# Kernel optimization log

Hardware: AMD Instinct MI355X
Metric: run time of the kernel (lower is better)

The kernel has to match this reference:

```python
import jax, jax.numpy as jnp
import numpy as np

D_MODEL = 1024
HEADS = 16
HEAD_DIM = D_MODEL // HEADS


def setup_inputs() -> dict:
    key = jax.random.key(0)
    ks = jax.random.split(key, 9)
    s = 1.0 / np.sqrt(D_MODEL)
    inp = {
        "inputs": jax.random.normal(ks[0], (4, 2048, D_MODEL), dtype=jnp.float32),
        "Wq": jax.random.normal(ks[1], (D_MODEL, D_MODEL), dtype=jnp.float32) * s,
        "bq": jnp.zeros((D_MODEL,), dtype=jnp.float32),
        "Wk": jax.random.normal(ks[2], (D_MODEL, D_MODEL), dtype=jnp.float32) * s,
        "bk": jnp.zeros((D_MODEL,), dtype=jnp.float32),
        "Wv": jax.random.normal(ks[3], (D_MODEL, D_MODEL), dtype=jnp.float32) * s,
        "bv": jnp.zeros((D_MODEL,), dtype=jnp.float32),
        "Wo": jax.random.normal(ks[4], (D_MODEL, D_MODEL), dtype=jnp.float32) * s,
        "bo": jnp.zeros((D_MODEL,), dtype=jnp.float32),
    }
    return inp


def reference(inputs, Wq, bq, Wk, bk, Wv, bv, Wo, bo):
    bs, seq, _ = inputs.shape
    # projections -> [b, h, s, d]
    def split_heads(x):
        return x.reshape(bs, seq, HEADS, HEAD_DIM).transpose(0, 2, 1, 3)
    q = split_heads(inputs @ Wq + bq)
    k = split_heads(inputs @ Wk + bk)
    v = split_heads(inputs @ Wv + bv)
    # NOTE: original code divides by (head_dim ** 1 / 2) == head_dim/2, not sqrt(head_dim)
    scale = HEAD_DIM / 2.0
    scores = jnp.einsum("bhqd,bhkd->bhqk", q, k) / scale
    attn = jax.nn.softmax(scores, axis=-1)
    out = jnp.einsum("bhqk,bhkd->bhqd", attn, v)
    out = out.transpose(0, 2, 1, 3).reshape(bs, seq, HEADS * HEAD_DIM)
    return out @ Wo + bo
```

## Files before the change

### kernel.cpp

```cpp
#include <hip/hip_runtime.h>
#include <stdint.h>

typedef __attribute__((ext_vector_type(8))) short bf16x8;
typedef __attribute__((ext_vector_type(4))) float f32x4;
typedef __attribute__((address_space(1))) void as1_void;
typedef __attribute__((address_space(3))) void as3_void;

#define D_MODEL 1024
#define SEQ     2048
#define BATCH   4
#define HEADS   16
#define HDIM    64

#define QSCALE 0.045084220029218407f

__device__ __forceinline__ ushort f2bf(float f) {
  union { float f; unsigned u; } v; v.f = f;
  unsigned u = v.u + 0x7fffu + ((v.u >> 16) & 1u);
  return (ushort)(u >> 16);
}

__device__ __forceinline__ void gload_lds16(const void* g, void* l) {
  __builtin_amdgcn_global_load_lds((as1_void*)(uintptr_t)g, (as3_void*)l, 16, 0, 0);
}

__device__ __forceinline__ bf16x8 pack8(float a0, float a1, float a2, float a3,
                                        float a4, float a5, float a6, float a7) {
  union { uint u[4]; bf16x8 v; } x;
  x.u[0] = __builtin_amdgcn_perm(__float_as_uint(a1), __float_as_uint(a0), 0x07060302);
  x.u[1] = __builtin_amdgcn_perm(__float_as_uint(a3), __float_as_uint(a2), 0x07060302);
  x.u[2] = __builtin_amdgcn_perm(__float_as_uint(a5), __float_as_uint(a4), 0x07060302);
  x.u[3] = __builtin_amdgcn_perm(__float_as_uint(a7), __float_as_uint(a6), 0x07060302);
  return x.v;
}

__global__ void prep_kernel(const float* __restrict__ X,
                            const float* w0, const float* w1, const float* w2, const float* w3,
                            const float* __restrict__ bq, const float* __restrict__ bk,
                            const float* __restrict__ bv,
                            ushort* __restrict__ Xb, ushort* __restrict__ WT,
                            float* __restrict__ bcat) {
  __shared__ float tile[32][33];
  const int bx = blockIdx.x, t = threadIdx.x;
  if (bx < 8192) {
    int i = bx * 256 + t;
    float4 f = reinterpret_cast<const float4*>(X)[i];
    ushort4 o;
    o.x = f2bf(f.x); o.y = f2bf(f.y); o.z = f2bf(f.z); o.w = f2bf(f.w);
    reinterpret_cast<ushort4*>(Xb)[i] = o;
  } else if (bx < 12288) {
    int tz = bx - 8192;
    int z = tz >> 10;
    int xy = tz & 1023;
    int bxt = xy & 31, byt = xy >> 5;
    const float* w = (z == 0) ? w0 : (z == 1) ? w1 : (z == 2) ? w2 : w3;
    const float sc = (z == 0) ? QSCALE : 1.0f;
    ushort* o = WT + (size_t)z * D_MODEL * D_MODEL;
    int tx = t & 31, ty = t >> 5;
    int x = bxt * 32 + tx;
    int y0 = byt * 32;
    #pragma unroll
    for (int i = ty; i < 32; i += 8)
      tile[i][tx] = w[(size_t)(y0 + i) * D_MODEL + x];
    __syncthreads();
    #pragma unroll
    for (int i = ty; i < 32; i += 8)
      o[(size_t)(bxt * 32 + i) * D_MODEL + y0 + tx] = f2bf(tile[tx][i] * sc);
  } else {
    int i = (bx - 12288) * 256 + t;
    bcat[i] = (i < 1024) ? bq[i] * QSCALE : (i < 2048) ? bk[i - 1024] : bv[i - 2048];
  }
}

#define MFMA16(a, b, c) __builtin_amdgcn_mfma_f32_16x16x32_bf16(a, b, c, 0, 0, 0)

__global__ __launch_bounds__(512, 2) void gemm_qkv(const ushort* __restrict__ A, const ushort* __restrict__ BT,
                                                   const float* __restrict__ bias,
                                                   ushort* __restrict__ QK, ushort* __restrict__ Vt) {
  __shared__ __align__(16) char smem[131072];
  const int tid  = threadIdx.x;
  const int w    = tid >> 6;
  const int lane = tid & 63;
  const int lo   = lane & 15, quad = lane >> 4;
  const int wr   = w >> 2, wc = w & 3;

  const int orig = blockIdx.y * 12 + blockIdx.x;
  const int wg   = (orig & 7) * 48 + (orig >> 3);
  const int m0   = (wg / 12) * 256;
  const int n0   = (wg % 12) * 256;

  const int tl = tid ^ ((tid >> 3) & 7);
  const ushort* sA = A  + (size_t)(m0 + (tl >> 3)) * 1024 + (tl & 7) * 8;
  const ushort* sB = BT + (size_t)(n0 + (tl >> 3)) * 1024 + (tl & 7) * 8;
  char* lw = smem + w * 1024;

  const int o0 = (quad * 16) ^ ((lo & 7) << 4);
  const int o1 = o0 ^ 64;
  const int rdA = wr * 16384 + lo * 128;
  const int rdB = 65536 + (wc * 64 + lo) * 128;

  f32x4 acc[8][4];
  #pragma unroll
  for (int i = 0; i < 8; ++i)
    #pragma unroll
    for (int j = 0; j < 4; ++j) acc[i][j] = {0.f, 0.f, 0.f, 0.f};

  gload_lds16(sB,              lw + 65536);
  gload_lds16(sB +  64 * 1024, lw + 65536 +  8192);
  gload_lds16(sB + 128 * 1024, lw + 65536 + 16384);
  gload_lds16(sB + 192 * 1024, lw + 65536 + 24576);
  gload_lds16(sA,              lw);
  gload_lds16(sA + 128 * 1024, lw + 16384);
  gload_lds16(sA +  64 * 1024, lw +  8192);
  gload_lds16(sA + 192 * 1024, lw + 24576);
  asm volatile("s_waitcnt vmcnt(2)" ::: "memory");
  __builtin_amdgcn_s_barrier();
  asm volatile("" ::: "memory");

  const char* L = smem;
  #pragma unroll 2
  for (int kt = 0; kt < 16; ++kt) {
    const int b32 = (kt & 1) << 15;
    const int nb  = b32 ^ 32768;
    const int kc  = (kt + 1) * 64;
    const bool pf = kt < 15;
    bf16x8 bfr[4][2], af0[2], af1[2];

    #pragma unroll
    for (int ni = 0; ni < 4; ++ni) {
      bfr[ni][0] = *(const bf16x8*)(L + b32 + rdB + ni * 2048 + o0);
      bfr[ni][1] = *(const bf16x8*)(L + b32 + rdB + ni * 2048 + o1);
    }
    af0[0] = *(const bf16x8*)(L + b32 + rdA + o0);
    af0[1] = *(const bf16x8*)(L + b32 + rdA + o1);
    af1[0] = *(const bf16x8*)(L + b32 + rdA + 2048 + o0);
    af1[1] = *(const bf16x8*)(L + b32 + rdA + 2048 + o1);
    if (pf) {
      gload_lds16(sB + kc,             lw + nb + 65536);
      gload_lds16(sB + 64 * 1024 + kc, lw + nb + 65536 + 8192);
    }
    asm volatile("s_waitcnt lgkmcnt(8)" ::: "memory");
    __builtin_amdgcn_s_barrier();
    asm volatile("s_waitcnt lgkmcnt(0)" ::: "memory");
    __builtin_amdgcn_sched_barrier(0);
    __builtin_amdgcn_s_setprio(1);
    #pragma unroll
    for (int ks = 0; ks < 2; ++ks)
      #pragma unroll
      for (int ni = 0; ni < 4; ++ni) {
        acc[0][ni] = MFMA16(af0[ks], bfr[ni][ks], acc[0][ni]);
        acc[1][ni] = MFMA16(af1[ks], bfr[ni][ks], acc[1][ni]);
      }
    __builtin_amdgcn_s_setprio(0);
    __builtin_amdgcn_s_barrier();
    asm volatile("" ::: "memory");

    af0[0] = *(const bf16x8*)(L + b32 + rdA + 2 * 2048 + o0);
    af0[1] = *(const bf16x8*)(L + b32 + rdA + 2 * 2048 + o1);
    af1[0] = *(const bf16x8*)(L + b32 + rdA + 3 * 2048 + o0);
    af1[1] = *(const bf16x8*)(L + b32 + rdA + 3 * 2048 + o1);
    if (pf) {
      gload_lds16(sB + 128 * 1024 + kc, lw + nb + 65536 + 16384);
      gload_lds16(sB + 192 * 1024 + kc, lw + nb + 65536 + 24576);
    }
    __builtin_amdgcn_s_barrier();
    asm volatile("s_waitcnt lgkmcnt(0)" ::: "memory");
    __builtin_amdgcn_sched_barrier(0);
    __builtin_amdgcn_s_setprio(1);
    #pragma unroll
    for (int ks = 0; ks < 2; ++ks)
      #pragma unroll
      for (int ni = 0; ni < 4; ++ni) {
        acc[2][ni] = MFMA16(af0[ks], bfr[ni][ks], acc[2][ni]);
        acc[3][ni] = MFMA16(af1[ks], bfr[ni][ks], acc[3][ni]);
      }
    __builtin_amdgcn_s_setprio(0);
    if (pf) asm volatile("s_waitcnt vmcnt(4)" ::: "memory");
    else    asm volatile("s_waitcnt vmcnt(0)" ::: "memory");
    __builtin_amdgcn_s_barrier();
    asm volatile("" ::: "memory");

    af0[0] = *(const bf16x8*)(L + b32 + rdA + 4 * 2048 + o0);
    af0[1] = *(const bf16x8*)(L + b32 + rdA + 4 * 2048 + o1);
    af1[0] = *(const bf16x8*)(L + b32 + rdA + 5 * 2048 + o0);
    af1[1] = *(const bf16x8*)(L + b32 + rdA + 5 * 2048 + o1);
    if (pf) {
      gload_lds16(sA + kc,              lw + nb);
      gload_lds16(sA + 128 * 1024 + kc, lw + nb + 16384);
    }
    __builtin_amdgcn_s_barrier();
    asm volatile("s_waitcnt lgkmcnt(0)" ::: "memory");
    __builtin_amdgcn_sched_barrier(0);
    __builtin_amdgcn_s_setprio(1);
    #pragma unroll
    for (int ks = 0; ks < 2; ++ks)
      #pragma unroll
      for (int ni = 0; ni < 4; ++ni) {
        acc[4][ni] = MFMA16(af0[ks], bfr[ni][ks], acc[4][ni]);
        acc[5][ni] = MFMA16(af1[ks], bfr[ni][ks], acc[5][ni]);
      }
    __builtin_amdgcn_s_setprio(0);
    __builtin_amdgcn_s_barrier();
    asm volatile("" ::: "memory");

    af0[0] = *(const bf16x8*)(L + b32 + rdA + 6 * 2048 + o0);
    af0[1] = *(const bf16x8*)(L + b32 + rdA + 6 * 2048 + o1);
    af1[0] = *(const bf16x8*)(L + b32 + rdA + 7 * 2048 + o0);
    af1[1] = *(const bf16x8*)(L + b32 + rdA + 7 * 2048 + o1);
    if (pf) {
      gload_lds16(sA + 64 * 1024 + kc,  lw + nb + 8192);
      gload_lds16(sA + 192 * 1024 + kc, lw + nb + 24576);
    }
    __builtin_amdgcn_s_barrier();
    asm volatile("s_waitcnt lgkmcnt(0)" ::: "memory");
    __builtin_amdgcn_sched_barrier(0);
    __builtin_amdgcn_s_setprio(1);
    #pragma unroll
    for (int ks = 0; ks < 2; ++ks)
      #pragma unroll
      for (int ni = 0; ni < 4; ++ni) {
        acc[6][ni] = MFMA16(af0[ks], bfr[ni][ks], acc[6][ni]);
        acc[7][ni] = MFMA16(af1[ks], bfr[ni][ks], acc[7][ni]);
      }
    __builtin_amdgcn_s_setprio(0);
    if (pf) asm volatile("s_waitcnt vmcnt(2)" ::: "memory");
    __builtin_amdgcn_s_barrier();
    asm volatile("" ::: "memory");
  }

  if (n0 < 2048) {
    #pragma unroll
    for (int ni = 0; ni < 4; ++ni) {
      const int col = n0 + wc * 64 + ni * 16 + lo;
      const float bv = bias[col];
      #pragma unroll
      for (int mi = 0; mi < 8; ++mi) {
        const int row = m0 + wr * 128 + mi * 16 + quad * 4;
        #pragma unroll
        for (int r = 0; r < 4; ++r)
          QK[(size_t)(row + r) * 2048 + col] = f2bf(acc[mi][ni][r] + bv);
      }
    }
  } else {
    #pragma unroll
    for (int ni = 0; ni < 4; ++ni) {
      const int col  = n0 + wc * 64 + ni * 16 + lo;
      const int vcol = col - 2048;
      const int hh = vcol >> 6, d = vcol & 63;
      const float bv = bias[col];
      #pragma unroll
      for (int mi = 0; mi < 8; ++mi) {
        const int base = m0 + wr * 128 + mi * 16;
        const int brow = base + quad * 4;
        const int bidx = brow >> 11;
        const int srow = brow & 2047;
        const int ck   = srow >> 6;
        const int c0   = (base & 32) + (quad << 3) + ((base >> 2) & 4);
        ushort e0 = f2bf(acc[mi][ni][0] + bv);
        ushort e1 = f2bf(acc[mi][ni][1] + bv);
        ushort e2 = f2bf(acc[mi][ni][2] + bv);
        ushort e3 = f2bf(acc[mi][ni][3] + bv);
        uint2 pk;
        pk.x = (uint)e0 | ((uint)e1 << 16);
        pk.y = (uint)e2 | ((uint)e3 << 16);
        *(uint2*)&Vt[(size_t)((bidx * HEADS + hh) * HDIM + d) * SEQ + ck * 64 + c0] = pk;
      }
    }
  }
}

__global__ __launch_bounds__(256) void gemm_bt_f32(const ushort* __restrict__ A, const ushort* __restrict__ BT,
                                                   const float* __restrict__ bias, float* __restrict__ C,
                                                   int M, int N, int K) {
  __shared__ __align__(16) ushort As[128 * 32];
  __shared__ __align__(16) ushort Bs[128 * 32];
  const int tid  = threadIdx.x;
  const int w    = tid >> 6;
  const int lane = tid & 63;
  const int lo   = lane & 15, quad = lane >> 4;
  const int m0 = blockIdx.y * 128, n0 = blockIdx.x * 128;
  const int ra = lane >> 2;
  const int ca = (lane & 3) * 8;
  const int wm = (w & 1) * 64, wn = (w >> 1) * 64;

  f32x4 acc[4][4];
  #pragma unroll
  for (int i = 0; i < 4; ++i)
    #pragma unroll
    for (int j = 0; j < 4; ++j) acc[i][j] = {0.f, 0.f, 0.f, 0.f};

  for (int k0 = 0; k0 < K; k0 += 32) {
    #pragma unroll
    for (int i = 0; i < 2; ++i) {
      const int j = w * 2 + i;
      gload_lds16(A  + (size_t)(m0 + j * 16 + ra) * K + k0 + ca, &As[j * 512]);
      gload_lds16(BT + (size_t)(n0 + j * 16 + ra) * K + k0 + ca, &Bs[j * 512]);
    }
    __syncthreads();
    bf16x8 af[4], bfv[4];
    #pragma unroll
    for (int mi = 0; mi < 4; ++mi) af[mi]  = *(const bf16x8*)&As[(wm + mi * 16 + lo) * 32 + quad * 8];
    #pragma unroll
    for (int ni = 0; ni < 4; ++ni) bfv[ni] = *(const bf16x8*)&Bs[(wn + ni * 16 + lo) * 32 + quad * 8];
    #pragma unroll
    for (int mi = 0; mi < 4; ++mi)
      #pragma unroll
      for (int ni = 0; ni < 4; ++ni)
        acc[mi][ni] = __builtin_amdgcn_mfma_f32_16x16x32_bf16(af[mi], bfv[ni], acc[mi][ni], 0, 0, 0);
    __syncthreads();
  }

  #pragma unroll
  for (int ni = 0; ni < 4; ++ni) {
    const int col = n0 + wn + ni * 16 + lo;
    const float bv = bias[col];
    #pragma unroll
    for (int mi = 0; mi < 4; ++mi) {
      #pragma unroll
      for (int r = 0; r < 4; ++r) {
        const int row = m0 + wm + mi * 16 + quad * 4 + r;
        C[(size_t)row * N + col] = acc[mi][ni][r] + bv;
      }
    }
  }
}

__global__ __launch_bounds__(256, 2) void attn_kernel(const ushort* __restrict__ QK,
                                                      const ushort* __restrict__ Vt,
                                                      ushort* __restrict__ Og) {
  __shared__ __align__(16) ushort Ks[2][64 * 64];
  __shared__ __align__(16) ushort Vs[2][64 * 64];

  const int tid  = threadIdx.x;
  const int w    = tid >> 6, lane = tid & 63;
  const int lo   = lane & 15, quad = lane >> 4;

  const int p  = blockIdx.x + (blockIdx.y << 3) + (blockIdx.z << 7);
  const int G  = ((p >> 6) << 3) | (p & 7);
  const int h  = G & 15, b = G >> 4;
  const int qbase = ((p >> 3) & 7) * 256 + w * 64;
  const int swz = lo & 7;

  auto STAGE = [&](int buf, int ck) {
    #pragma unroll
    for (int i = 0; i < 2; ++i) {
      const int c16 = (w * 2 + i) * 64 + lane;
      const int r = c16 >> 3, ps = c16 & 7;
      const int gs = ps ^ (r & 7);
      gload_lds16(QK + (size_t)(b * SEQ + ck * 64 + r) * 2048 + 1024 + h * HDIM + gs * 8,
                  &Ks[buf][(w * 2 + i) * 512]);
      gload_lds16(Vt + (size_t)((b * HEADS + h) * HDIM + r) * SEQ + ck * 64 + gs * 8,
                  &Vs[buf][(w * 2 + i) * 512]);
    }
  };

  bf16x8 qf[4][2];
  #pragma unroll
  for (int qg = 0; qg < 4; ++qg) {
    const ushort* qp = QK + (size_t)(b * SEQ + qbase + qg * 16 + lo) * 2048 + h * HDIM;
    qf[qg][0] = *(const bf16x8*)(qp + quad * 8);
    qf[qg][1] = *(const bf16x8*)(qp + 32 + quad * 8);
  }

  f32x4 acc[4][4];
  #pragma unroll
  for (int qg = 0; qg < 4; ++qg)
    #pragma unroll
    for (int t = 0; t < 4; ++t) acc[qg][t] = {0.f, 0.f, 0.f, 0.f};
  float lsum[4] = {0.f, 0.f, 0.f, 0.f};

  STAGE(0, 0);
  __syncthreads();

  #pragma unroll 2
  for (int ck = 0; ck < SEQ / 64; ++ck) {
    const int cur = ck & 1;
    if (ck < SEQ / 64 - 1) {
      STAGE(cur ^ 1, ck + 1);
      asm volatile("s_waitcnt vmcnt(4)" ::: "memory");
    } else {
      asm volatile("s_waitcnt vmcnt(0)" ::: "memory");
    }
    __builtin_amdgcn_s_barrier();
    asm volatile("" ::: "memory");

    bf16x8 kf[4][2];
    #pragma unroll
    for (int sub = 0; sub < 4; ++sub) {
      const ushort* kr = &Ks[cur][(sub * 16 + lo) * 64];
      kf[sub][0] = *(const bf16x8*)(kr + ((quad ^ swz) * 8));
      kf[sub][1] = *(const bf16x8*)(kr + (((4 + quad) ^ swz) * 8));
    }

    bf16x8 af[4][2];
    #pragma unroll
    for (int qg = 0; qg < 4; ++qg) {
      f32x4 s[4];
      #pragma unroll
      for (int sub = 0; sub < 4; ++sub) s[sub] = {0.f, 0.f, 0.f, 0.f};
      #pragma unroll
      for (int sub = 0; sub < 4; ++sub) {
        s[sub] = __builtin_amdgcn_mfma_f32_16x16x32_bf16(kf[sub][0], qf[qg][0], s[sub], 0, 0, 0);
        s[sub] = __builtin_amdgcn_mfma_f32_16x16x32_bf16(kf[sub][1], qf[qg][1], s[sub], 0, 0, 0);
      }
      float p2[4][4];
      #pragma unroll
      for (int sub = 0; sub < 4; ++sub)
        #pragma unroll
        for (int r = 0; r < 4; ++r) p2[sub][r] = __builtin_amdgcn_exp2f(s[sub][r]);
      float t0 = 0.f;
      #pragma unroll
      for (int sub = 0; sub < 4; ++sub)
        t0 += (p2[sub][0] + p2[sub][1]) + (p2[sub][2] + p2[sub][3]);
      lsum[qg] += t0;
      af[qg][0] = pack8(p2[0][0], p2[0][1], p2[0][2], p2[0][3], p2[1][0], p2[1][1], p2[1][2], p2[1][3]);
      af[qg][1] = pack8(p2[2][0], p2[2][1], p2[2][2], p2[2][3], p2[3][0], p2[3][1], p2[3][2], p2[3][3]);
    }

    __builtin_amdgcn_s_setprio(1);
    #pragma unroll
    for (int t = 0; t < 4; ++t) {
      const ushort* vr = &Vs[cur][(t * 16 + lo) * 64];
      #pragma unroll
      for (int hh = 0; hh < 2; ++hh) {
        bf16x8 vf = *(const bf16x8*)(vr + (((hh * 4 + quad) ^ swz) * 8));
        #pragma unroll
        for (int qg = 0; qg < 4; ++qg)
          acc[qg][t] = __builtin_amdgcn_mfma_f32_16x16x32_bf16(af[qg][hh], vf, acc[qg][t], 0, 0, 0);
      }
    }
    __builtin_amdgcn_s_setprio(0);

    asm volatile("" ::: "memory");
    __builtin_amdgcn_s_barrier();
    asm volatile("" ::: "memory");
  }

  #pragma unroll
  for (int qg = 0; qg < 4; ++qg) {
    float v = lsum[qg];
    v += __shfl_xor(v, 16);
    v += __shfl_xor(v, 32);
    float linv[4];
    #pragma unroll
    for (int r = 0; r < 4; ++r) linv[r] = 1.0f / __shfl(v, quad * 4 + r);
    #pragma unroll
    for (int t = 0; t < 4; ++t)
      #pragma unroll
      for (int r = 0; r < 4; ++r)
        Og[(size_t)(b * SEQ + qbase + qg * 16 + quad * 4 + r) * D_MODEL + h * HDIM + t * 16 + lo] =
            f2bf(acc[qg][t][r] * linv[r]);
  }
}

extern "C" void kernel_launch(void* const* d_in, const int* in_sizes, int n_in,
                              void* d_out, int out_size, void* d_ws, size_t ws_size,
                              hipStream_t stream) {
  const float* X  = (const float*)d_in[0];
  const float* Wq = (const float*)d_in[1];
  const float* bq = (const float*)d_in[2];
  const float* Wk = (const float*)d_in[3];
  const float* bk = (const float*)d_in[4];
  const float* Wv = (const float*)d_in[5];
  const float* bv = (const float*)d_in[6];
  const float* Wo = (const float*)d_in[7];
  const float* bo = (const float*)d_in[8];
  float* out = (float*)d_out;
  char* ws = (char*)d_ws;

  ushort* Xb  = (ushort*)(ws);
  ushort* WT  = (ushort*)(ws + 16777216);
  ushort* QKb = (ushort*)(ws + 25165824);
  ushort* Vtb = (ushort*)(ws + 58720256);
  ushort* Ob  = (ushort*)(ws + 75497472);
  float*  bcat = (float*)(ws + 75497472);
  const int WSTRIDE = D_MODEL * D_MODEL;

  prep_kernel<<<12300, 256, 0, stream>>>(X, Wq, Wk, Wv, Wo, bq, bk, bv, Xb, WT, bcat);

  gemm_qkv<<<dim3(12, 32), 512, 0, stream>>>(Xb, WT, bcat, QKb, Vtb);

  attn_kernel<<<dim3(SEQ / 256, HEADS, BATCH), 256, 0, stream>>>(QKb, Vtb, Ob);

  gemm_bt_f32<<<dim3(8, 64), 256, 0, stream>>>(Ob, WT + 3 * WSTRIDE, bo, out,
                                               BATCH * SEQ, D_MODEL, D_MODEL);
}
```

Before: 260.6 us.

## Template 8-wave pipelined GEMM over N tile; reuse for QKV and output projection

Turns the hand-pipelined QKV GEMM into a template parameterized by N-tile width and output type. The QKV projection now uses 256x192 tiles, giving 512 workgroups instead of 384 for better CU balance. The output projection drops the simple 128x128 single-buffered kernel and uses the 256x128 double-buffered pipelined variant with fp32 output. The prefetch schedule is reworked per tile width, which risks wait-count mismatches, and the 192-wide tile lowers per-block reuse.

```diff
diff --git a/kernel.cpp b/kernel.cpp
--- a/kernel.cpp
+++ b/kernel.cpp
@@ -74,45 +74,54 @@
 
 #define MFMA16(a, b, c) __builtin_amdgcn_mfma_f32_16x16x32_bf16(a, b, c, 0, 0, 0)
 
-__global__ __launch_bounds__(512, 2) void gemm_qkv(const ushort* __restrict__ A, const ushort* __restrict__ BT,
-                                                   const float* __restrict__ bias,
-                                                   ushort* __restrict__ QK, ushort* __restrict__ Vt) {
-  __shared__ __align__(16) char smem[131072];
+template <int BN, bool F32OUT>
+__global__ __launch_bounds__(512, 2) void gemm8p(const ushort* __restrict__ A,
+                                                 const ushort* __restrict__ BT,
+                                                 const float* __restrict__ bias,
+                                                 ushort* __restrict__ QK,
+                                                 ushort* __restrict__ Vt,
+                                                 float* __restrict__ Cf) {
+  constexpr int NI = BN / 64;
+  constexpr int BB = BN * 128;
+  constexpr int WCOL = BN / 4;
+  __shared__ __align__(16) char smem[65536 + 2 * BB];
   const int tid  = threadIdx.x;
   const int w    = tid >> 6;
   const int lane = tid & 63;
   const int lo   = lane & 15, quad = lane >> 4;
   const int wr   = w >> 2, wc = w & 3;
 
-  const int orig = blockIdx.y * 12 + blockIdx.x;
-  const int wg   = (orig & 7) * 48 + (orig >> 3);
-  const int m0   = (wg / 12) * 256;
-  const int n0   = (wg % 12) * 256;
+  const int nx   = gridDim.x;
+  const int nwg  = nx * gridDim.y;
+  const int orig = blockIdx.y * nx + blockIdx.x;
+  const int wg   = (orig & 7) * (nwg >> 3) + (orig >> 3);
+  const int m0   = (wg / nx) * 256;
+  const int n0   = (wg % nx) * BN;
 
   const int tl = tid ^ ((tid >> 3) & 7);
   const ushort* sA = A  + (size_t)(m0 + (tl >> 3)) * 1024 + (tl & 7) * 8;
   const ushort* sB = BT + (size_t)(n0 + (tl >> 3)) * 1024 + (tl & 7) * 8;
-  char* lw = smem + w * 1024;
+  char* lwA = smem + w * 1024;
+  char* lwB = smem + 65536 + w * 1024;
 
   const int o0 = (quad * 16) ^ ((lo & 7) << 4);
   const int o1 = o0 ^ 64;
   const int rdA = wr * 16384 + lo * 128;
-  const int rdB = 65536 + (wc * 64 + lo) * 128;
-
-  f32x4 acc[8][4];
+  const int rdB = 65536 + (wc * WCOL + lo) * 128;
+
+  f32x4 acc[8][NI];
   #pragma unroll
   for (int i = 0; i < 8; ++i)
     #pragma unroll
-    for (int j = 0; j < 4; ++j) acc[i][j] = {0.f, 0.f, 0.f, 0.f};
-
-  gload_lds16(sB,              lw + 65536);
-  gload_lds16(sB +  64 * 1024, lw + 65536 +  8192);
-  gload_lds16(sB + 128 * 1024, lw + 65536 + 16384);
-  gload_lds16(sB + 192 * 1024, lw + 65536 + 24576);
-  gload_lds16(sA,              lw);
-  gload_lds16(sA + 128 * 1024, lw + 16384);
-  gload_lds16(sA +  64 * 1024, lw +  8192);
-  gload_lds16(sA + 192 * 1024, lw + 24576);
+    for (int j = 0; j < NI; ++j) acc[i][j] = {0.f, 0.f, 0.f, 0.f};
+
+  gload_lds16(sB,               lwB);
+  gload_lds16(sB +  64 * 1024,  lwB +  8192);
+  if constexpr (NI == 3) gload_lds16(sB + 128 * 1024, lwB + 16384);
+  gload_lds16(sA,               lwA);
+  gload_lds16(sA + 128 * 1024,  lwA + 16384);
+  gload_lds16(sA +  64 * 1024,  lwA +  8192);
+  gload_lds16(sA + 192 * 1024,  lwA + 24576);
   asm volatile("s_waitcnt vmcnt(2)" ::: "memory");
   __builtin_amdgcn_s_barrier();
   asm volatile("" ::: "memory");
@@ -120,24 +129,26 @@
   const char* L = smem;
   #pragma unroll 2
   for (int kt = 0; kt < 16; ++kt) {
-    const int b32 = (kt & 1) << 15;
-    const int nb  = b32 ^ 32768;
-    const int kc  = (kt + 1) * 64;
-    const bool pf = kt < 15;
-    bf16x8 bfr[4][2], af0[2], af1[2];
-
-    #pragma unroll
-    for (int ni = 0; ni < 4; ++ni) {
-      bfr[ni][0] = *(const bf16x8*)(L + b32 + rdB + ni * 2048 + o0);
-      bfr[ni][1] = *(const bf16x8*)(L + b32 + rdB + ni * 2048 + o1);
-    }
-    af0[0] = *(const bf16x8*)(L + b32 + rdA + o0);
-    af0[1] = *(const bf16x8*)(L + b32 + rdA + o1);
-    af1[0] = *(const bf16x8*)(L + b32 + rdA + 2048 + o0);
-    af1[1] = *(const bf16x8*)(L + b32 + rdA + 2048 + o1);
+    const int b32A = (kt & 1) << 15;
+    const int b32B = (kt & 1) * BB;
+    const int nbA  = b32A ^ 32768;
+    const int nbB  = b32B ^ BB;
+    const int kc   = (kt + 1) * 64;
+    const bool pf  = kt < 15;
+    bf16x8 bfr[NI][2], af0[2], af1[2];
+
+    #pragma unroll
+    for (int ni = 0; ni < NI; ++ni) {
+      bfr[ni][0] = *(const bf16x8*)(L + b32B + rdB + ni * 2048 + o0);
+      bfr[ni][1] = *(const bf16x8*)(L + b32B + rdB + ni * 2048 + o1);
+    }
+    af0[0] = *(const bf16x8*)(L + b32A + rdA + o0);
+    af0[1] = *(const bf16x8*)(L + b32A + rdA + o1);
+    af1[0] = *(const bf16x8*)(L + b32A + rdA + 2048 + o0);
+    af1[1] = *(const bf16x8*)(L + b32A + rdA + 2048 + o1);
     if (pf) {
-      gload_lds16(sB + kc,             lw + nb + 65536);
-      gload_lds16(sB + 64 * 1024 + kc, lw + nb + 65536 + 8192);
+      gload_lds16(sB + kc,             lwB + nbB);
+      gload_lds16(sB + 64 * 1024 + kc, lwB + nbB + 8192);
     }
     asm volatile("s_waitcnt lgkmcnt(8)" ::: "memory");
     __builtin_amdgcn_s_barrier();
@@ -147,7 +158,7 @@
     #pragma unroll
     for (int ks = 0; ks < 2; ++ks)
       #pragma unroll
-      for (int ni = 0; ni < 4; ++ni) {
+      for (int ni = 0; ni < NI; ++ni) {
         acc[0][ni] = MFMA16(af0[ks], bfr[ni][ks], acc[0][ni]);
         acc[1][ni] = MFMA16(af1[ks], bfr[ni][ks], acc[1][ni]);
       }
@@ -155,13 +166,18 @@
     __builtin_amdgcn_s_barrier();
     asm volatile("" ::: "memory");
 
-    af0[0] = *(const bf16x8*)(L + b32 + rdA + 2 * 2048 + o0);
-    af0[1] = *(const bf16x8*)(L + b32 + rdA + 2 * 2048 + o1);
-    af1[0] = *(const bf16x8*)(L + b32 + rdA + 3 * 2048 + o0);
-    af1[1] = *(const bf16x8*)(L + b32 + rdA + 3 * 2048 + o1);
+    af0[0] = *(const bf16x8*)(L + b32A + rdA + 2 * 2048 + o0);
+    af0[1] = *(const bf16x8*)(L + b32A + rdA + 2 * 2048 + o1);
+    af1[0] = *(const bf16x8*)(L + b32A + rdA + 3 * 2048 + o0);
+    af1[1] = *(const bf16x8*)(L + b32A + rdA + 3 * 2048 + o1);
     if (pf) {
-      gload_lds16(sB + 128 * 1024 + kc, lw + nb + 65536 + 16384);
-      gload_lds16(sB + 192 * 1024 + kc, lw + nb + 65536 + 24576);
+      if constexpr (NI == 3) {
+        gload_lds16(sB + 128 * 1024 + kc, lwB + nbB + 16384);
+        gload_lds16(sA + kc,              lwA + nbA);
+      } else {
+        gload_lds16(sA + kc,              lwA + nbA);
+        gload_lds16(sA + 128 * 1024 + kc, lwA + nbA + 16384);
+      }
     }
     __builtin_amdgcn_s_barrier();
     asm volatile("s_waitcnt lgkmcnt(0)" ::: "memory");
@@ -170,7 +186,7 @@
     #pragma unroll
     for (int ks = 0; ks < 2; ++ks)
       #pragma unroll
-      for (int ni = 0; ni < 4; ++ni) {
+      for (int ni = 0; ni < NI; ++ni) {
         acc[2][ni] = MFMA16(af0[ks], bfr[ni][ks], acc[2][ni]);
         acc[3][ni] = MFMA16(af1[ks], bfr[ni][ks], acc[3][ni]);
       }
@@ -180,13 +196,15 @@
     __builtin_amdgcn_s_barrier();
     asm volatile("" ::: "memory");
 
-    af0[0] = *(const bf16x8*)(L + b32 + rdA + 4 * 2048 + o0);
-    af0[1] = *(const bf16x8*)(L + b32 + rdA + 4 * 2048 + o1);
-    af1[0] = *(const bf16x8*)(L + b32 + rdA + 5 * 2048 + o0);
-    af1[1] = *(const bf16x8*)(L + b32 + rdA + 5 * 2048 + o1);
+    af0[0] = *(const bf16x8*)(L + b32A + rdA + 4 * 2048 + o0);
+    af0[1] = *(const bf16x8*)(L + b32A + rdA + 4 * 2048 + o1);
+    af1[0] = *(const bf16x8*)(L + b32A + rdA + 5 * 2048 + o0);
+    af1[1] = *(const bf16x8*)(L + b32A + rdA + 5 * 2048 + o1);
     if (pf) {
-      gload_lds16(sA + kc,              lw + nb);
-      gload_lds16(sA + 128 * 1024 + kc, lw + nb + 16384);
+      if constexpr (NI == 3)
+        gload_lds16(sA + 128 * 1024 + kc, lwA + nbA + 16384);
+      else
+        gload_lds16(sA + 64 * 1024 + kc,  lwA + nbA + 8192);
     }
     __builtin_amdgcn_s_barrier();
     asm volatile("s_waitcnt lgkmcnt(0)" ::: "memory");
@@ -195,7 +213,7 @@
     #pragma unroll
     for (int ks = 0; ks < 2; ++ks)
       #pragma unroll
-      for (int ni = 0; ni < 4; ++ni) {
+      for (int ni = 0; ni < NI; ++ni) {
         acc[4][ni] = MFMA16(af0[ks], bfr[ni][ks], acc[4][ni]);
         acc[5][ni] = MFMA16(af1[ks], bfr[ni][ks], acc[5][ni]);
       }
@@ -203,13 +221,17 @@
     __builtin_amdgcn_s_barrier();
     asm volatile("" ::: "memory");
 
-    af0[0] = *(const bf16x8*)(L + b32 + rdA + 6 * 2048 + o0);
-    af0[1] = *(const bf16x8*)(L + b32 + rdA + 6 * 2048 + o1);
-    af1[0] = *(const bf16x8*)(L + b32 + rdA + 7 * 2048 + o0);
-    af1[1] = *(const bf16x8*)(L + b32 + rdA + 7 * 2048 + o1);
+    af0[0] = *(const bf16x8*)(L + b32A + rdA + 6 * 2048 + o0);
+    af0[1] = *(const bf16x8*)(L + b32A + rdA + 6 * 2048 + o1);
+    af1[0] = *(const bf16x8*)(L + b32A + rdA + 7 * 2048 + o0);
+    af1[1] = *(const bf16x8*)(L + b32A + rdA + 7 * 2048 + o1);
     if (pf) {
-      gload_lds16(sA + 64 * 1024 + kc,  lw + nb + 8192);
-      gload_lds16(sA + 192 * 1024 + kc, lw + nb + 24576);
+      if constexpr (NI == 3) {
+        gload_lds16(sA + 64 * 1024 + kc,  lwA + nbA + 8192);
+        gload_lds16(sA + 192 * 1024 + kc, lwA + nbA + 24576);
+      } else {
+        gload_lds16(sA + 192 * 1024 + kc, lwA + nbA + 24576);
+      }
     }
     __builtin_amdgcn_s_barrier();
     asm volatile("s_waitcnt lgkmcnt(0)" ::: "memory");
@@ -218,7 +240,7 @@
     #pragma unroll
     for (int ks = 0; ks < 2; ++ks)
       #pragma unroll
-      for (int ni = 0; ni < 4; ++ni) {
+      for (int ni = 0; ni < NI; ++ni) {
         acc[6][ni] = MFMA16(af0[ks], bfr[ni][ks], acc[6][ni]);
         acc[7][ni] = MFMA16(af1[ks], bfr[ni][ks], acc[7][ni]);
       }
@@ -228,98 +250,53 @@
     asm volatile("" ::: "memory");
   }
 
-  if (n0 < 2048) {
-    #pragma unroll
-    for (int ni = 0; ni < 4; ++ni) {
-      const int col = n0 + wc * 64 + ni * 16 + lo;
+  if constexpr (F32OUT) {
+    #pragma unroll
+    for (int ni = 0; ni < NI; ++ni) {
+      const int col = n0 + wc * WCOL + ni * 16 + lo;
       const float bv = bias[col];
       #pragma unroll
       for (int mi = 0; mi < 8; ++mi) {
         const int row = m0 + wr * 128 + mi * 16 + quad * 4;
         #pragma unroll
         for (int r = 0; r < 4; ++r)
-          QK[(size_t)(row + r) * 2048 + col] = f2bf(acc[mi][ni][r] + bv);
+          Cf[(size_t)(row + r) * 1024 + col] = acc[mi][ni][r] + bv;
       }
     }
   } else {
     #pragma unroll
-    for (int ni = 0; ni < 4; ++ni) {
-      const int col  = n0 + wc * 64 + ni * 16 + lo;
-      const int vcol = col - 2048;
-      const int hh = vcol >> 6, d = vcol & 63;
-      const float bv = bias[col];
-      #pragma unroll
-      for (int mi = 0; mi < 8; ++mi) {
-        const int base = m0 + wr * 128 + mi * 16;
-        const int brow = base + quad * 4;
-        const int bidx = brow >> 11;
-        const int srow = brow & 2047;
-        const int ck   = srow >> 6;
-        const int c0   = (base & 32) + (quad << 3) + ((base >> 2) & 4);
-        ushort e0 = f2bf(acc[mi][ni][0] + bv);
-        ushort e1 = f2bf(acc[mi][ni][1] + bv);
-        ushort e2 = f2bf(acc[mi][ni][2] + bv);
-        ushort e3 = f2bf(acc[mi][ni][3] + bv);
-        uint2 pk;
-        pk.x = (uint)e0 | ((uint)e1 << 16);
-        pk.y = (uint)e2 | ((uint)e3 << 16);
-        *(uint2*)&Vt[(size_t)((bidx * HEADS + hh) * HDIM + d) * SEQ + ck * 64 + c0] = pk;
-      }
-    }
-  }
-}
-
-__global__ __launch_bounds__(256) void gemm_bt_f32(const ushort* __restrict__ A, const ushort* __restrict__ BT,
-                                                   const float* __restrict__ bias, float* __restrict__ C,
-                                                   int M, int N, int K) {
-  __shared__ __align__(16) ushort As[128 * 32];
-  __shared__ __align__(16) ushort Bs[128 * 32];
-  const int tid  = threadIdx.x;
-  const int w    = tid >> 6;
-  const int lane = tid & 63;
-  const int lo   = lane & 15, quad = lane >> 4;
-  const int m0 = blockIdx.y * 128, n0 = blockIdx.x * 128;
-  const int ra = lane >> 2;
-  const int ca = (lane & 3) * 8;
-  const int wm = (w & 1) * 64, wn = (w >> 1) * 64;
-
-  f32x4 acc[4][4];
-  #pragma unroll
-  for (int i = 0; i < 4; ++i)
-    #pragma unroll
-    for (int j = 0; j < 4; ++j) acc[i][j] = {0.f, 0.f, 0.f, 0.f};
-
-  for (int k0 = 0; k0 < K; k0 += 32) {
-    #pragma unroll
-    for (int i = 0; i < 2; ++i) {
-      const int j = w * 2 + i;
-      gload_lds16(A  + (size_t)(m0 + j * 16 + ra) * K + k0 + ca, &As[j * 512]);
-      gload_lds16(BT + (size_t)(n0 + j * 16 + ra) * K + k0 + ca, &Bs[j * 512]);
-    }
-    __syncthreads();
-    bf16x8 af[4], bfv[4];
-    #pragma unroll
-    for (int mi = 0; mi < 4; ++mi) af[mi]  = *(const bf16x8*)&As[(wm + mi * 16 + lo) * 32 + quad * 8];
-    #pragma unroll
-    for (int ni = 0; ni < 4; ++ni) bfv[ni] = *(const bf16x8*)&Bs[(wn + ni * 16 + lo) * 32 + quad * 8];
-    #pragma unroll
-    for (int mi = 0; mi < 4; ++mi)
-      #pragma unroll
-      for (int ni = 0; ni < 4; ++ni)
-        acc[mi][ni] = __builtin_amdgcn_mfma_f32_16x16x32_bf16(af[mi], bfv[ni], acc[mi][ni], 0, 0, 0);
-    __syncthreads();
-  }
-
-  #pragma unroll
-  for (int ni = 0; ni < 4; ++ni) {
-    const int col = n0 + wn + ni * 16 + lo;
-    const float bv = bias[col];
-    #pragma unroll
-    for (int mi = 0; mi < 4; ++mi) {
-      #pragma unroll
-      for (int r = 0; r < 4; ++r) {
-        const int row = m0 + wm + mi * 16 + quad * 4 + r;
-        C[(size_t)row * N + col] = acc[mi][ni][r] + bv;
+    for (int ni = 0; ni < NI; ++ni) {
+      const int colb = n0 + wc * WCOL + ni * 16;
+      const float bv = bias[colb + lo];
+      if (colb < 2048) {
+        const int col = colb + lo;
+        #pragma unroll
+        for (int mi = 0; mi < 8; ++mi) {
+          const int row = m0 + wr * 128 + mi * 16 + quad * 4;
+          #pragma unroll
+          for (int r = 0; r < 4; ++r)
+            QK[(size_t)(row + r) * 2048 + col] = f2bf(acc[mi][ni][r] + bv);
+        }
+      } else {
+        const int vcol = colb + lo - 2048;
+        const int hh = vcol >> 6, d = vcol & 63;
+        #pragma unroll
+        for (int mi = 0; mi < 8; ++mi) {
+          const int base = m0 + wr * 128 + mi * 16;
+          const int brow = base + quad * 4;
+          const int bidx = brow >> 11;
+          const int srow = brow & 2047;
+          const int ck   = srow >> 6;
+          const int c0   = (base & 32) + (quad << 3) + ((base >> 2) & 4);
+          ushort e0 = f2bf(acc[mi][ni][0] + bv);
+          ushort e1 = f2bf(acc[mi][ni][1] + bv);
+          ushort e2 = f2bf(acc[mi][ni][2] + bv);
+          ushort e3 = f2bf(acc[mi][ni][3] + bv);
+          uint2 pk;
+          pk.x = (uint)e0 | ((uint)e1 << 16);
+          pk.y = (uint)e2 | ((uint)e3 << 16);
+          *(uint2*)&Vt[(size_t)((bidx * HEADS + hh) * HDIM + d) * SEQ + ck * 64 + c0] = pk;
+        }
       }
     }
   }
@@ -478,10 +455,9 @@
 
   prep_kernel<<<12300, 256, 0, stream>>>(X, Wq, Wk, Wv, Wo, bq, bk, bv, Xb, WT, bcat);
 
-  gemm_qkv<<<dim3(12, 32), 512, 0, stream>>>(Xb, WT, bcat, QKb, Vtb);
+  gemm8p<192, false><<<dim3(16, 32), 512, 0, stream>>>(Xb, WT, bcat, QKb, Vtb, nullptr);
 
   attn_kernel<<<dim3(SEQ / 256, HEADS, BATCH), 256, 0, stream>>>(QKb, Vtb, Ob);
 
-  gemm_bt_f32<<<dim3(8, 64), 256, 0, stream>>>(Ob, WT + 3 * WSTRIDE, bo, out,
-                                               BATCH * SEQ, D_MODEL, D_MODEL);
-}
+  gemm8p<128, true><<<dim3(8, 32), 512, 0, stream>>>(Ob, WT + 3 * WSTRIDE, bo, nullptr, nullptr, out);
+}
```

Measured after the change: 249.9 us. -4.1%, faster.
